# Kernel tuning notes

Measured on AMD Instinct MI355X. Metric: run time of the kernel, lower is better.

Reference implementation:

```python
import jax, jax.numpy as jnp
import numpy as np

N_NODES = 100000
K = 10
LAMBDA_AMP = 0.5
GAMMA = 1.0 / (2.0 * (1.0 - LAMBDA_AMP))


def setup_inputs() -> dict:
    key = jax.random.key(0)
    ks = jax.random.split(key, 6)
    x = jax.random.normal(ks[0], (N_NODES, 500), dtype=jnp.float32)
    W1 = jax.random.normal(ks[1], (500, 256), dtype=jnp.float32) * (1.0 / np.sqrt(500))
    b1 = jnp.zeros((256,), dtype=jnp.float32)
    W2 = jax.random.normal(ks[2], (256, 40), dtype=jnp.float32) * (1.0 / np.sqrt(256))
    b2 = jnp.zeros((40,), dtype=jnp.float32)
    edge_src = jax.random.randint(ks[3], (1600000,), 0, N_NODES, dtype=jnp.int32)
    edge_dst = jax.random.randint(ks[4], (1600000,), 0, N_NODES, dtype=jnp.int32)
    return {"x": x, "W1": W1, "b1": b1, "W2": W2, "b2": b2,
            "edge_src": edge_src, "edge_dst": edge_dst}


def _amp(h, src, dst, wn):
    """AdaptiveMessagePassing.amp_forward: K iterations of SpMM + L21 proximal."""
    hh = h
    xk = h
    coef = GAMMA * 2.0 * (1.0 - LAMBDA_AMP)  # == 1.0 by construction
    lam = GAMMA * LAMBDA_AMP
    score = jnp.zeros((h.shape[0],), h.dtype)
    for _ in range(K):
        # propagate: A_norm @ xk  (segment-sum SpMM over edge list)
        prop = jax.ops.segment_sum(wn[:, None] * xk[src], dst, num_segments=h.shape[0])
        lx = xk - prop                     # compute_LX
        y = xk - coef * lx
        diff = y - hh
        # proximal_L21
        rn = jnp.sqrt(jnp.sum(diff * diff, axis=1))   # [N]
        score = jnp.maximum(rn - lam, 0.0)
        rn_safe = jnp.where(rn > 0, rn, 1.0)
        score = jnp.where(rn > 0, score / rn_safe, score)
        xk = hh + score[:, None] * diff
    return xk, score


def reference(x, W1, b1, W2, b2, edge_src, edge_dst):
    N = x.shape[0]
    # MLP (eval mode -> dropout is identity)
    h = jax.nn.relu(x @ W1 + b1)
    h = h @ W2 + b2                                   # [N, C]
    # gcn_norm with self-loops, symmetric D^-1/2 A D^-1/2
    loop = jnp.arange(N, dtype=edge_src.dtype)
    src = jnp.concatenate([edge_src, loop])
    dst = jnp.concatenate([edge_dst, loop])
    w = jnp.ones(src.shape[0], dtype=h.dtype)
    deg = jax.ops.segment_sum(w, dst, num_segments=N)
    dinv = jnp.where(deg > 0, jax.lax.rsqrt(jnp.where(deg > 0, deg, 1.0)), 0.0)
    wn = dinv[src] * w * dinv[dst]
    out, score = _amp(h, src, dst, wn)
    return jax.nn.log_softmax(out, axis=1), score
```

## Files before the change

kernel.cpp:

```cpp
#include <hip/hip_runtime.h>
#include <math.h>

#define NF 500
#define KPAD 512
#define NH 256
#define NC 40
#define P0 32
#define P1 8
#define KIT 10
#define LAMW 0.5f

typedef __attribute__((ext_vector_type(8))) short short8;
typedef __attribute__((ext_vector_type(4))) float f32x4;

__device__ __forceinline__ unsigned short bf_rne(float v) {
    unsigned int b = __float_as_uint(v);
    unsigned int h = (b + 0x7FFFu + ((b >> 16) & 1u)) >> 16;
    return (unsigned short)h;
}

__global__ void w1prep_kernel(const float* __restrict__ W1, unsigned short* __restrict__ H,
                              unsigned short* __restrict__ L) {
    int k = blockIdx.x;
    int c = threadIdx.x;
    float v = (k < NF) ? W1[(size_t)k * NH + c] : 0.f;
    unsigned short h = bf_rne(v);
    float hf = __uint_as_float(((unsigned int)h) << 16);
    unsigned short lo = bf_rne(v - hf);
    H[(size_t)c * KPAD + k] = h;
    L[(size_t)c * KPAD + k] = lo;
}
__global__ void w2prep_kernel(const float* __restrict__ W2, unsigned short* __restrict__ H,
                              unsigned short* __restrict__ L) {
    int c = blockIdx.x;
    int k = threadIdx.x;
    float v = (c < NC) ? W2[(size_t)k * NC + c] : 0.f;
    unsigned short h = bf_rne(v);
    float hf = __uint_as_float(((unsigned int)h) << 16);
    unsigned short lo = bf_rne(v - hf);
    H[(size_t)c * NH + k] = h;
    L[(size_t)c * NH + k] = lo;
}

__device__ __forceinline__ void mlp_load_tile(const float* __restrict__ xrow, int gr, int N,
                                              int skof, int tt, float v[8]) {
    if (gr < N && tt < 15) {
        float4 a = *(const float4*)(xrow + tt * 32);
        float4 b = *(const float4*)(xrow + tt * 32 + 4);
        v[0]=a.x; v[1]=a.y; v[2]=a.z; v[3]=a.w; v[4]=b.x; v[5]=b.y; v[6]=b.z; v[7]=b.w;
    } else {
        #pragma unroll
        for (int j = 0; j < 8; j++) {
            int k = tt * 32 + skof + j;
            v[j] = (gr < N && k < NF) ? xrow[tt * 32 + j] : 0.f;
        }
    }
}

__global__ __launch_bounds__(256, 4) void mlp_mfma_kernel(
    const float* __restrict__ x, const float* __restrict__ b1,
    const unsigned short* __restrict__ W1tH, const unsigned short* __restrict__ W1tL,
    const unsigned short* __restrict__ W2tH, const unsigned short* __restrict__ W2tL,
    const float* __restrict__ b2, float* __restrict__ hp0, float* __restrict__ hp1, int N)
{
    __shared__ unsigned short smem[17408];
    unsigned short* Hhi = smem;
    unsigned short* Hlo = smem + 64 * 136;

    const int t   = threadIdx.x;
    const int w   = t >> 6;
    const int l   = t & 63;
    const int l15 = l & 15;
    const int lq  = l >> 4;
    const int row0 = blockIdx.x * 64;

    f32x4 acc[4][4];
    #pragma unroll
    for (int r = 0; r < 4; r++)
        #pragma unroll
        for (int c = 0; c < 4; c++) acc[r][c] = (f32x4){0.f, 0.f, 0.f, 0.f};

    const int srow = t >> 2;
    const int skof = (t & 3) * 8;
    const int gr = row0 + srow;
    const float* xrow = x + (size_t)gr * NF + skof;

    float v_cur[8], v_nxt[8], v_p[8];
    mlp_load_tile(xrow, gr, N, skof, 0, v_cur);
    mlp_load_tile(xrow, gr, N, skof, 1, v_nxt);

    {
        short8 sh, sl;
        #pragma unroll
        for (int j = 0; j < 8; j++) {
            unsigned int b = __float_as_uint(v_cur[j]);
            unsigned int h = (b + 0x7FFFu + ((b >> 16) & 1u)) >> 16;
            float hf = __uint_as_float(h << 16);
            float rr = v_cur[j] - hf;
            unsigned int rb = __float_as_uint(rr);
            unsigned int lo = (rb + 0x7FFFu + ((rb >> 16) & 1u)) >> 16;
            sh[j] = (short)h; sl[j] = (short)lo;
        }
        *(short8*)&smem[srow * 40 + skof] = sh;
        *(short8*)&smem[2560 + srow * 40 + skof] = sl;
    }
    __syncthreads();

    const size_t bB = (size_t)(64 * w + l15) * KPAD + lq * 8;
    for (int kt = 0; kt < 16; ++kt) {
        const int cur = kt & 1;
        short8 ah[4], al[4], bh[4], bl[4];
        #pragma unroll
        for (int r = 0; r < 4; r++) {
            ah[r] = *(short8*)&smem[cur * 5120 + (16 * r + l15) * 40 + lq * 8];
            al[r] = *(short8*)&smem[cur * 5120 + 2560 + (16 * r + l15) * 40 + lq * 8];
        }
        #pragma unroll
        for (int c = 0; c < 4; c++) {
            bh[c] = *(const short8*)&W1tH[bB + (size_t)c * 16 * KPAD + kt * 32];
            bl[c] = *(const short8*)&W1tL[bB + (size_t)c * 16 * KPAD + kt * 32];
        }
        if (kt < 14) mlp_load_tile(xrow, gr, N, skof, kt + 2, v_p);
        if (kt < 15) {
            short8 sh, sl;
            #pragma unroll
            for (int j = 0; j < 8; j++) {
                unsigned int b = __float_as_uint(v_nxt[j]);
                unsigned int h = (b + 0x7FFFu + ((b >> 16) & 1u)) >> 16;
                float hf = __uint_as_float(h << 16);
                float rr = v_nxt[j] - hf;
                unsigned int rb = __float_as_uint(rr);
                unsigned int lo = (rb + 0x7FFFu + ((rb >> 16) & 1u)) >> 16;
                sh[j] = (short)h; sl[j] = (short)lo;
            }
            *(short8*)&smem[(cur ^ 1) * 5120 + srow * 40 + skof] = sh;
            *(short8*)&smem[(cur ^ 1) * 5120 + 2560 + srow * 40 + skof] = sl;
        }
        #pragma unroll
        for (int c = 0; c < 4; c++)
            #pragma unroll
            for (int r = 0; r < 4; r++) {
                acc[r][c] = __builtin_amdgcn_mfma_f32_16x16x32_bf16(ah[r], bh[c], acc[r][c], 0, 0, 0);
                acc[r][c] = __builtin_amdgcn_mfma_f32_16x16x32_bf16(al[r], bh[c], acc[r][c], 0, 0, 0);
                acc[r][c] = __builtin_amdgcn_mfma_f32_16x16x32_bf16(ah[r], bl[c], acc[r][c], 0, 0, 0);
            }
        __syncthreads();
        if (kt < 14) {
            #pragma unroll
            for (int j = 0; j < 8; j++) v_nxt[j] = v_p[j];
        }
    }

    f32x4 acc2[3];
    #pragma unroll
    for (int cf = 0; cf < 3; cf++) acc2[cf] = (f32x4){0.f, 0.f, 0.f, 0.f};

    #pragma unroll
    for (int hf2 = 0; hf2 < 2; ++hf2) {
        if ((w >> 1) == hf2) {
            #pragma unroll
            for (int c = 0; c < 4; c++) {
                int lcol = 64 * (w & 1) + 16 * c + l15;
                float bb = b1[64 * w + 16 * c + l15];
                #pragma unroll
                for (int r = 0; r < 4; r++) {
                    #pragma unroll
                    for (int g = 0; g < 4; g++) {
                        float hval = fmaxf(acc[r][c][g] + bb, 0.f);
                        unsigned int hb = __float_as_uint(hval);
                        unsigned int h = (hb + 0x7FFFu + ((hb >> 16) & 1u)) >> 16;
                        float hff = __uint_as_float(h << 16);
                        float rr = hval - hff;
                        unsigned int rb = __float_as_uint(rr);
                        unsigned int lo = (rb + 0x7FFFu + ((rb >> 16) & 1u)) >> 16;
                        int rowi = 16 * r + lq * 4 + g;
                        Hhi[rowi * 136 + lcol] = (unsigned short)h;
                        Hlo[rowi * 136 + lcol] = (unsigned short)lo;
                    }
                }
            }
        }
        __syncthreads();
        const int hbase = (16 * w + l15) * 136 + lq * 8;
        const int wbase = l15 * NH + 128 * hf2 + lq * 8;
        #pragma unroll
        for (int kt = 0; kt < 4; ++kt) {
            short8 bhf = *(short8*)&Hhi[hbase + kt * 32];
            short8 blf = *(short8*)&Hlo[hbase + kt * 32];
            #pragma unroll
            for (int cf = 0; cf < 3; cf++) {
                short8 awh = *(const short8*)&W2tH[wbase + cf * 16 * NH + kt * 32];
                short8 awl = *(const short8*)&W2tL[wbase + cf * 16 * NH + kt * 32];
                acc2[cf] = __builtin_amdgcn_mfma_f32_16x16x32_bf16(awh, bhf, acc2[cf], 0, 0, 0);
                acc2[cf] = __builtin_amdgcn_mfma_f32_16x16x32_bf16(awl, bhf, acc2[cf], 0, 0, 0);
                acc2[cf] = __builtin_amdgcn_mfma_f32_16x16x32_bf16(awh, blf, acc2[cf], 0, 0, 0);
            }
        }
        __syncthreads();
    }

    int node = row0 + 16 * w + l15;
    if (node < N) {
        #pragma unroll
        for (int cf = 0; cf < 3; cf++) {
            #pragma unroll
            for (int g = 0; g < 4; g++) {
                int cls = 16 * cf + lq * 4 + g;
                if (cls < P0) hp0[(size_t)node * P0 + cls] = acc2[cf][g] + b2[cls];
                else if (cls < NC) hp1[(size_t)node * P1 + (cls - P0)] = acc2[cf][g] + b2[cls];
            }
        }
    }
}

__global__ void zero_int_kernel(int* p, int N) {
    int i = blockIdx.x * 256 + threadIdx.x;
    if (i < N) p[i] = 0;
}
__global__ void cnt_edges_kernel(const int* __restrict__ dst, int* cnt, int E) {
    int e = blockIdx.x * 256 + threadIdx.x;
    if (e < E) atomicAdd(&cnt[dst[e]], 1);
}
__global__ void dinv_kernel(const int* __restrict__ cnt, float* dinv, int N) {
    int i = blockIdx.x * 256 + threadIdx.x;
    if (i < N) dinv[i] = rsqrtf((float)cnt[i] + 1.0f);
}
__global__ __launch_bounds__(1024) void scanA_kernel(
    const int* __restrict__ cnt, int* __restrict__ rowptr, int* __restrict__ bsum, int N)
{
    __shared__ int sd[1024];
    int t = threadIdx.x;
    int i = blockIdx.x * 1024 + t;
    sd[t] = (i < N) ? (cnt[i] + 1) : 0;
    __syncthreads();
    for (int off = 1; off < 1024; off <<= 1) {
        int v = (t >= off) ? sd[t - off] : 0;
        __syncthreads();
        if (t >= off) sd[t] += v;
        __syncthreads();
    }
    if (i < N) rowptr[i + 1] = sd[t];
    if (t == 1023) bsum[blockIdx.x] = sd[1023];
}
__global__ void scanB_kernel(int* bsum, int nb) {
    __shared__ int sb[256];
    int t = threadIdx.x;
    sb[t] = (t < nb) ? bsum[t] : 0;
    __syncthreads();
    if (t == 0) { int run = 0; for (int i = 0; i < nb; i++) { int v = sb[i]; sb[i] = run; run += v; } }
    __syncthreads();
    if (t < nb) bsum[t] = sb[t];
}
__global__ __launch_bounds__(1024) void scanC_kernel(int* rowptr, const int* __restrict__ bpre, int N) {
    int i = blockIdx.x * 1024 + threadIdx.x;
    if (i < N) rowptr[i + 1] += bpre[blockIdx.x];
    if (i == 0) rowptr[0] = 0;
}
__global__ void self_fill_kernel(const int* __restrict__ rowptr, const float* __restrict__ dinv,
                                 int2* __restrict__ csre, int* __restrict__ cursor, int N) {
    int i = blockIdx.x * 256 + threadIdx.x;
    if (i < N) {
        int p = rowptr[i];
        float d = dinv[i];
        csre[p] = make_int2(i, __float_as_int(d * d));
        cursor[i] = p + 1;
    }
}
__global__ void fill_csr_kernel(const int* __restrict__ src, const int* __restrict__ dst,
    const float* __restrict__ dinv, int* cursor, int2* __restrict__ csre, int E)
{
    int e = blockIdx.x * 256 + threadIdx.x;
    if (e < E) {
        int d = dst[e], s = src[e];
        int p = atomicAdd(&cursor[d], 1);
        csre[p] = make_int2(s, __float_as_int(dinv[s] * dinv[d]));
    }
}

__global__ __launch_bounds__(256, 8) void amp4_kernel(
    const float* __restrict__ xp0, const float* __restrict__ xp1,
    const float* __restrict__ hp0, const float* __restrict__ hp1,
    const int* __restrict__ rowptr, const int2* __restrict__ csre,
    float* __restrict__ np0, float* __restrict__ np1,
    float* __restrict__ lsm_out, float* __restrict__ score_out, int N, int last)
{
    const int n = (blockIdx.x * 256 + threadIdx.x) >> 6;
    if (n >= N) return;
    const int l = threadIdx.x & 63;
    const int g = l >> 3;
    const int j = l & 7;

    const int e0 = rowptr[n];
    const int e1 = rowptr[n + 1];
    const int em = e1 - 1;

    float ax = 0.f, ay = 0.f, az = 0.f, aw = 0.f, a5 = 0.f;
    for (int base = e0; base < e1; base += 16) {
        int ea = base + g;
        int eb = base + 8 + g;
        bool va = ea < e1;
        bool vb = eb < e1;
        int2 pa = csre[va ? ea : em];
        int2 pb = csre[vb ? eb : em];
        const float4 ra = *(const float4*)(xp0 + ((size_t)pa.x << 5) + (j << 2));
        const float4 rb = *(const float4*)(xp0 + ((size_t)pb.x << 5) + (j << 2));
        float sa = xp1[((size_t)pa.x << 3) + j];
        float sb = xp1[((size_t)pb.x << 3) + j];
        float wa = va ? __int_as_float(pa.y) : 0.f;
        float wb = vb ? __int_as_float(pb.y) : 0.f;
        ax += wa * ra.x + wb * rb.x;
        ay += wa * ra.y + wb * rb.y;
        az += wa * ra.z + wb * rb.z;
        aw += wa * ra.w + wb * rb.w;
        a5 += wa * sa + wb * sb;
    }
    ax += __shfl_xor(ax, 8);  ay += __shfl_xor(ay, 8);
    az += __shfl_xor(az, 8);  aw += __shfl_xor(aw, 8);  a5 += __shfl_xor(a5, 8);
    ax += __shfl_xor(ax, 16); ay += __shfl_xor(ay, 16);
    az += __shfl_xor(az, 16); aw += __shfl_xor(aw, 16); a5 += __shfl_xor(a5, 16);
    ax += __shfl_xor(ax, 32); ay += __shfl_xor(ay, 32);
    az += __shfl_xor(az, 32); aw += __shfl_xor(aw, 32); a5 += __shfl_xor(a5, 32);

    const float4 h4 = *(const float4*)(hp0 + ((size_t)n << 5) + (j << 2));
    const float h5 = hp1[((size_t)n << 3) + j];
    float dx = ax - h4.x, dy = ay - h4.y, dz = az - h4.z, dw = aw - h4.w, d5 = a5 - h5;
    float d2 = dx * dx + dy * dy + dz * dz + dw * dw + d5 * d5;
    d2 += __shfl_xor(d2, 1); d2 += __shfl_xor(d2, 2); d2 += __shfl_xor(d2, 4);

    float rn = sqrtf(d2);
    float sc = (rn > LAMW) ? (rn - LAMW) / rn : 0.f;
    float4 xn;
    xn.x = h4.x + sc * dx; xn.y = h4.y + sc * dy;
    xn.z = h4.z + sc * dz; xn.w = h4.w + sc * dw;
    float x5 = h5 + sc * d5;

    if (!last) {
        if (g == 0) {
            *(float4*)(np0 + ((size_t)n << 5) + (j << 2)) = xn;
            np1[((size_t)n << 3) + j] = x5;
        }
    } else {
        if (l == 0) score_out[n] = sc;
        float m = fmaxf(fmaxf(fmaxf(xn.x, xn.y), fmaxf(xn.z, xn.w)), x5);
        m = fmaxf(m, __shfl_xor(m, 1));
        m = fmaxf(m, __shfl_xor(m, 2));
        m = fmaxf(m, __shfl_xor(m, 4));
        float es = expf(xn.x - m) + expf(xn.y - m) + expf(xn.z - m)
                 + expf(xn.w - m) + expf(x5 - m);
        es += __shfl_xor(es, 1); es += __shfl_xor(es, 2); es += __shfl_xor(es, 4);
        float lse = m + logf(es);
        if (g == 0) {
            float4 o;
            o.x = xn.x - lse; o.y = xn.y - lse; o.z = xn.z - lse; o.w = xn.w - lse;
            *(float4*)(lsm_out + (size_t)n * NC + (j << 2)) = o;
            lsm_out[(size_t)n * NC + P0 + j] = x5 - lse;
        }
    }
}

extern "C" void kernel_launch(void* const* d_in, const int* in_sizes, int n_in,
                              void* d_out, int out_size, void* d_ws, size_t ws_size,
                              hipStream_t stream)
{
    const float* x  = (const float*)d_in[0];
    const float* W1 = (const float*)d_in[1];
    const float* b1 = (const float*)d_in[2];
    const float* W2 = (const float*)d_in[3];
    const float* b2 = (const float*)d_in[4];
    const int* esrc = (const int*)d_in[5];
    const int* edst = (const int*)d_in[6];
    const int N = in_sizes[0] / NF;
    const int E = in_sizes[5];

    char* W = (char*)d_ws;
    size_t o = 0;
    float* hh0 = (float*)(W + o); o += (size_t)N * P0 * 4;
    float* hh1 = (float*)(W + o); o += (size_t)N * P1 * 4;
    float* a0  = (float*)(W + o); o += (size_t)N * P0 * 4;
    float* a1  = (float*)(W + o); o += (size_t)N * P1 * 4;
    float* c0  = (float*)(W + o); o += (size_t)N * P0 * 4;
    float* c1  = (float*)(W + o); o += (size_t)N * P1 * 4;
    float* dinv = (float*)(W + o); o += (size_t)N * 4;
    int* rowptr = (int*)(W + o);   o += (size_t)(N + 1) * 4;
    int* cnt    = (int*)(W + o);   o += (size_t)N * 4;
    int* bsum   = (int*)(W + o);   o += 256 * 4;
    o = (o + 15) & ~(size_t)15;
    int2* csre  = (int2*)(W + o);  o += (size_t)(E + N) * 8;
    o = (o + 15) & ~(size_t)15;
    unsigned short* W1tH = (unsigned short*)(W + o); o += (size_t)NH * KPAD * 2;
    unsigned short* W1tL = (unsigned short*)(W + o); o += (size_t)NH * KPAD * 2;
    unsigned short* W2tH = (unsigned short*)(W + o); o += (size_t)48 * NH * 2;
    unsigned short* W2tL = (unsigned short*)(W + o); o += (size_t)48 * NH * 2;

    float* lsm = (float*)d_out;
    float* sco = lsm + (size_t)N * NC;

    const int gb = (N + 255) / 256;
    const int ge = (E + 255) / 256;
    const int nb = (N + 1023) / 1024;

    w1prep_kernel<<<KPAD, NH, 0, stream>>>(W1, W1tH, W1tL);
    w2prep_kernel<<<48, NH, 0, stream>>>(W2, W2tH, W2tL);
    mlp_mfma_kernel<<<(N + 63) / 64, 256, 0, stream>>>(x, b1, W1tH, W1tL, W2tH, W2tL, b2, hh0, hh1, N);

    zero_int_kernel<<<gb, 256, 0, stream>>>(cnt, N);
    cnt_edges_kernel<<<ge, 256, 0, stream>>>(edst, cnt, E);
    dinv_kernel<<<gb, 256, 0, stream>>>(cnt, dinv, N);
    scanA_kernel<<<nb, 1024, 0, stream>>>(cnt, rowptr, bsum, N);
    scanB_kernel<<<1, 256, 0, stream>>>(bsum, nb);
    scanC_kernel<<<nb, 1024, 0, stream>>>(rowptr, bsum, N);
    self_fill_kernel<<<gb, 256, 0, stream>>>(rowptr, dinv, csre, cnt, N);
    fill_csr_kernel<<<ge, 256, 0, stream>>>(esrc, edst, dinv, cnt, csre, E);

    const float* xo0 = hh0;
    const float* xo1 = hh1;
    float* b0[2] = {a0, c0};
    float* b1p[2] = {a1, c1};
    for (int k = 0; k < KIT; k++) {
        int last = (k == KIT - 1);
        float* n0 = b0[k & 1];
        float* n1 = b1p[k & 1];
        amp4_kernel<<<(N + 3) / 4, 256, 0, stream>>>(
            xo0, xo1, hh0, hh1, rowptr, csre, n0, n1, lsm, sco, N, last);
        xo0 = n0; xo1 = n1;
    }
}
```

Measured before the change: 1.311 ms.

## Store propagated node features in fp16 with padded 64-wide rows

The iterate features gathered in each SpMM iteration now live in a single fp16 array padded to 64 columns, replacing the split fp32 32+8 layout. Each lane loads one 16-byte vector per neighbour instead of a float4 plus a scalar, which roughly halves the bytes per gathered row and removes the second uncoalesced load. The fixed anchor h stays in fp32 at 64 columns and the MLP writes both copies. Rounding the iterate to fp16 on every iteration adds precision error that may compound over the ten steps. The MLP launch bound was also lowered from 4 to 2 blocks per CU.

```diff
diff --git a/kernel.cpp b/kernel.cpp
--- a/kernel.cpp
+++ b/kernel.cpp
@@ -1,12 +1,11 @@
 #include <hip/hip_runtime.h>
+#include <hip/hip_fp16.h>
 #include <math.h>
 
 #define NF 500
 #define KPAD 512
 #define NH 256
 #define NC 40
-#define P0 32
-#define P1 8
 #define KIT 10
 #define LAMW 0.5f
 
@@ -57,11 +56,11 @@
     }
 }
 
-__global__ __launch_bounds__(256, 4) void mlp_mfma_kernel(
+__global__ __launch_bounds__(256, 2) void mlp_mfma_kernel(
     const float* __restrict__ x, const float* __restrict__ b1,
     const unsigned short* __restrict__ W1tH, const unsigned short* __restrict__ W1tL,
     const unsigned short* __restrict__ W2tH, const unsigned short* __restrict__ W2tL,
-    const float* __restrict__ b2, float* __restrict__ hp0, float* __restrict__ hp1, int N)
+    const float* __restrict__ b2, float* __restrict__ hh, __half* __restrict__ xh0, int N)
 {
     __shared__ unsigned short smem[17408];
     unsigned short* Hhi = smem;
@@ -201,14 +200,22 @@
 
     int node = row0 + 16 * w + l15;
     if (node < N) {
+        size_t ob = (size_t)node << 6;
         #pragma unroll
         for (int cf = 0; cf < 3; cf++) {
             #pragma unroll
             for (int g = 0; g < 4; g++) {
                 int cls = 16 * cf + lq * 4 + g;
-                if (cls < P0) hp0[(size_t)node * P0 + cls] = acc2[cf][g] + b2[cls];
-                else if (cls < NC) hp1[(size_t)node * P1 + (cls - P0)] = acc2[cf][g] + b2[cls];
+                float val = (cls < NC) ? (acc2[cf][g] + b2[cls]) : 0.f;
+                hh[ob + cls] = val;
+                xh0[ob + cls] = __float2half(val);
             }
+        }
+        #pragma unroll
+        for (int g = 0; g < 4; g++) {
+            int p = 48 + lq * 4 + g;
+            hh[ob + p] = 0.f;
+            xh0[ob + p] = __float2half(0.f);
         }
     }
 }
@@ -277,12 +284,11 @@
     }
 }
 
-__global__ __launch_bounds__(256, 8) void amp4_kernel(
-    const float* __restrict__ xp0, const float* __restrict__ xp1,
-    const float* __restrict__ hp0, const float* __restrict__ hp1,
+__global__ __launch_bounds__(256, 8) void amp5_kernel(
+    const __half* __restrict__ xk, const float* __restrict__ hh,
     const int* __restrict__ rowptr, const int2* __restrict__ csre,
-    float* __restrict__ np0, float* __restrict__ np1,
-    float* __restrict__ lsm_out, float* __restrict__ score_out, int N, int last)
+    __half* __restrict__ xk_new, float* __restrict__ lsm_out,
+    float* __restrict__ score_out, int N, int last)
 {
     const int n = (blockIdx.x * 256 + threadIdx.x) >> 6;
     if (n >= N) return;
@@ -294,7 +300,10 @@
     const int e1 = rowptr[n + 1];
     const int em = e1 - 1;
 
-    float ax = 0.f, ay = 0.f, az = 0.f, aw = 0.f, a5 = 0.f;
+    float acc[8];
+    #pragma unroll
+    for (int i = 0; i < 8; i++) acc[i] = 0.f;
+
     for (int base = e0; base < e1; base += 16) {
         int ea = base + g;
         int eb = base + 8 + g;
@@ -302,58 +311,78 @@
         bool vb = eb < e1;
         int2 pa = csre[va ? ea : em];
         int2 pb = csre[vb ? eb : em];
-        const float4 ra = *(const float4*)(xp0 + ((size_t)pa.x << 5) + (j << 2));
-        const float4 rb = *(const float4*)(xp0 + ((size_t)pb.x << 5) + (j << 2));
-        float sa = xp1[((size_t)pa.x << 3) + j];
-        float sb = xp1[((size_t)pb.x << 3) + j];
+        const uint4 qa = *(const uint4*)(xk + ((size_t)pa.x << 6) + (j << 3));
+        const uint4 qb = *(const uint4*)(xk + ((size_t)pb.x << 6) + (j << 3));
         float wa = va ? __int_as_float(pa.y) : 0.f;
         float wb = vb ? __int_as_float(pb.y) : 0.f;
-        ax += wa * ra.x + wb * rb.x;
-        ay += wa * ra.y + wb * rb.y;
-        az += wa * ra.z + wb * rb.z;
-        aw += wa * ra.w + wb * rb.w;
-        a5 += wa * sa + wb * sb;
-    }
-    ax += __shfl_xor(ax, 8);  ay += __shfl_xor(ay, 8);
-    az += __shfl_xor(az, 8);  aw += __shfl_xor(aw, 8);  a5 += __shfl_xor(a5, 8);
-    ax += __shfl_xor(ax, 16); ay += __shfl_xor(ay, 16);
-    az += __shfl_xor(az, 16); aw += __shfl_xor(aw, 16); a5 += __shfl_xor(a5, 16);
-    ax += __shfl_xor(ax, 32); ay += __shfl_xor(ay, 32);
-    az += __shfl_xor(az, 32); aw += __shfl_xor(aw, 32); a5 += __shfl_xor(a5, 32);
-
-    const float4 h4 = *(const float4*)(hp0 + ((size_t)n << 5) + (j << 2));
-    const float h5 = hp1[((size_t)n << 3) + j];
-    float dx = ax - h4.x, dy = ay - h4.y, dz = az - h4.z, dw = aw - h4.w, d5 = a5 - h5;
-    float d2 = dx * dx + dy * dy + dz * dz + dw * dw + d5 * d5;
+        const unsigned int ua[4] = {qa.x, qa.y, qa.z, qa.w};
+        const unsigned int ub[4] = {qb.x, qb.y, qb.z, qb.w};
+        #pragma unroll
+        for (int q = 0; q < 4; q++) {
+            float2 fa = __half22float2(*reinterpret_cast<const __half2*>(&ua[q]));
+            float2 fb = __half22float2(*reinterpret_cast<const __half2*>(&ub[q]));
+            acc[2*q]   += wa * fa.x + wb * fb.x;
+            acc[2*q+1] += wa * fa.y + wb * fb.y;
+        }
+    }
+    #pragma unroll
+    for (int off = 8; off <= 32; off <<= 1) {
+        #pragma unroll
+        for (int i = 0; i < 8; i++) acc[i] += __shfl_xor(acc[i], off);
+    }
+
+    const float* hrow = hh + ((size_t)n << 6) + (j << 3);
+    float4 h0 = *(const float4*)hrow;
+    float4 h1 = *(const float4*)(hrow + 4);
+    float hv[8] = {h0.x, h0.y, h0.z, h0.w, h1.x, h1.y, h1.z, h1.w};
+    float diff[8], d2 = 0.f;
+    #pragma unroll
+    for (int i = 0; i < 8; i++) { diff[i] = acc[i] - hv[i]; d2 += diff[i] * diff[i]; }
     d2 += __shfl_xor(d2, 1); d2 += __shfl_xor(d2, 2); d2 += __shfl_xor(d2, 4);
 
     float rn = sqrtf(d2);
     float sc = (rn > LAMW) ? (rn - LAMW) / rn : 0.f;
-    float4 xn;
-    xn.x = h4.x + sc * dx; xn.y = h4.y + sc * dy;
-    xn.z = h4.z + sc * dz; xn.w = h4.w + sc * dw;
-    float x5 = h5 + sc * d5;
+    float xn[8];
+    #pragma unroll
+    for (int i = 0; i < 8; i++) xn[i] = hv[i] + sc * diff[i];
 
     if (!last) {
         if (g == 0) {
-            *(float4*)(np0 + ((size_t)n << 5) + (j << 2)) = xn;
-            np1[((size_t)n << 3) + j] = x5;
+            uint4 qo;
+            __half2 p0 = __floats2half2_rn(xn[0], xn[1]);
+            __half2 p1 = __floats2half2_rn(xn[2], xn[3]);
+            __half2 p2 = __floats2half2_rn(xn[4], xn[5]);
+            __half2 p3 = __floats2half2_rn(xn[6], xn[7]);
+            qo.x = *reinterpret_cast<unsigned int*>(&p0);
+            qo.y = *reinterpret_cast<unsigned int*>(&p1);
+            qo.z = *reinterpret_cast<unsigned int*>(&p2);
+            qo.w = *reinterpret_cast<unsigned int*>(&p3);
+            *(uint4*)(xk_new + ((size_t)n << 6) + (j << 3)) = qo;
         }
     } else {
         if (l == 0) score_out[n] = sc;
-        float m = fmaxf(fmaxf(fmaxf(xn.x, xn.y), fmaxf(xn.z, xn.w)), x5);
+        bool real = (j < 5);
+        float m = -3.4e38f;
+        if (real) {
+            #pragma unroll
+            for (int i = 0; i < 8; i++) m = fmaxf(m, xn[i]);
+        }
         m = fmaxf(m, __shfl_xor(m, 1));
         m = fmaxf(m, __shfl_xor(m, 2));
         m = fmaxf(m, __shfl_xor(m, 4));
-        float es = expf(xn.x - m) + expf(xn.y - m) + expf(xn.z - m)
-                 + expf(xn.w - m) + expf(x5 - m);
+        float es = 0.f;
+        if (real) {
+            #pragma unroll
+            for (int i = 0; i < 8; i++) es += expf(xn[i] - m);
+        }
         es += __shfl_xor(es, 1); es += __shfl_xor(es, 2); es += __shfl_xor(es, 4);
         float lse = m + logf(es);
-        if (g == 0) {
-            float4 o;
-            o.x = xn.x - lse; o.y = xn.y - lse; o.z = xn.z - lse; o.w = xn.w - lse;
-            *(float4*)(lsm_out + (size_t)n * NC + (j << 2)) = o;
-            lsm_out[(size_t)n * NC + P0 + j] = x5 - lse;
+        if (g == 0 && real) {
+            float4 o0, o1;
+            o0.x = xn[0] - lse; o0.y = xn[1] - lse; o0.z = xn[2] - lse; o0.w = xn[3] - lse;
+            o1.x = xn[4] - lse; o1.y = xn[5] - lse; o1.z = xn[6] - lse; o1.w = xn[7] - lse;
+            *(float4*)(lsm_out + (size_t)n * NC + (j << 3)) = o0;
+            *(float4*)(lsm_out + (size_t)n * NC + (j << 3) + 4) = o1;
         }
     }
 }
@@ -374,18 +403,15 @@
 
     char* W = (char*)d_ws;
     size_t o = 0;
-    float* hh0 = (float*)(W + o); o += (size_t)N * P0 * 4;
-    float* hh1 = (float*)(W + o); o += (size_t)N * P1 * 4;
-    float* a0  = (float*)(W + o); o += (size_t)N * P0 * 4;
-    float* a1  = (float*)(W + o); o += (size_t)N * P1 * 4;
-    float* c0  = (float*)(W + o); o += (size_t)N * P0 * 4;
-    float* c1  = (float*)(W + o); o += (size_t)N * P1 * 4;
-    float* dinv = (float*)(W + o); o += (size_t)N * 4;
-    int* rowptr = (int*)(W + o);   o += (size_t)(N + 1) * 4;
-    int* cnt    = (int*)(W + o);   o += (size_t)N * 4;
-    int* bsum   = (int*)(W + o);   o += 256 * 4;
+    float* hh    = (float*)(W + o);  o += (size_t)N * 64 * 4;
+    __half* xhX  = (__half*)(W + o); o += (size_t)N * 64 * 2;
+    __half* xhA  = (__half*)(W + o); o += (size_t)N * 64 * 2;
+    float* dinv  = (float*)(W + o);  o += (size_t)N * 4;
+    int* rowptr  = (int*)(W + o);    o += (size_t)(N + 1) * 4;
+    int* cnt     = (int*)(W + o);    o += (size_t)N * 4;
+    int* bsum    = (int*)(W + o);    o += 256 * 4;
     o = (o + 15) & ~(size_t)15;
-    int2* csre  = (int2*)(W + o);  o += (size_t)(E + N) * 8;
+    int2* csre   = (int2*)(W + o);   o += (size_t)(E + N) * 8;
     o = (o + 15) & ~(size_t)15;
     unsigned short* W1tH = (unsigned short*)(W + o); o += (size_t)NH * KPAD * 2;
     unsigned short* W1tL = (unsigned short*)(W + o); o += (size_t)NH * KPAD * 2;
@@ -401,7 +427,7 @@
 
     w1prep_kernel<<<KPAD, NH, 0, stream>>>(W1, W1tH, W1tL);
     w2prep_kernel<<<48, NH, 0, stream>>>(W2, W2tH, W2tL);
-    mlp_mfma_kernel<<<(N + 63) / 64, 256, 0, stream>>>(x, b1, W1tH, W1tL, W2tH, W2tL, b2, hh0, hh1, N);
+    mlp_mfma_kernel<<<(N + 63) / 64, 256, 0, stream>>>(x, b1, W1tH, W1tL, W2tH, W2tL, b2, hh, xhX, N);
 
     zero_int_kernel<<<gb, 256, 0, stream>>>(cnt, N);
     cnt_edges_kernel<<<ge, 256, 0, stream>>>(edst, cnt, E);
@@ -412,16 +438,13 @@
     self_fill_kernel<<<gb, 256, 0, stream>>>(rowptr, dinv, csre, cnt, N);
     fill_csr_kernel<<<ge, 256, 0, stream>>>(esrc, edst, dinv, cnt, csre, E);
 
-    const float* xo0 = hh0;
-    const float* xo1 = hh1;
-    float* b0[2] = {a0, c0};
-    float* b1p[2] = {a1, c1};
+    const __half* xold = xhX;
+    __half* bufs[2] = {xhA, xhX};
     for (int k = 0; k < KIT; k++) {
         int last = (k == KIT - 1);
-        float* n0 = b0[k & 1];
-        float* n1 = b1p[k & 1];
-        amp4_kernel<<<(N + 3) / 4, 256, 0, stream>>>(
-            xo0, xo1, hh0, hh1, rowptr, csre, n0, n1, lsm, sco, N, last);
-        xo0 = n0; xo1 = n1;
-    }
-}
+        __half* xnew = bufs[k & 1];
+        amp5_kernel<<<(N + 3) / 4, 256, 0, stream>>>(
+            xold, hh, rowptr, csre, xnew, lsm, sco, N, last);
+        xold = xnew;
+    }
+}
```

After: 1.050 ms. 19.9% less time.
